# Performance work log

Measured on AMD Instinct MI355X. Metric: run time of the kernel, lower is better.

Reference implementation:

```python
import jax, jax.numpy as jnp
import numpy as np

D = 256
N = 8192
M = 8192


def setup_inputs() -> dict:
    key = jax.random.key(0)
    k1, k2, k3 = jax.random.split(key, 3)
    query = jax.random.normal(k1, (N, D), dtype=jnp.float32)
    context = jax.random.normal(k2, (M, D), dtype=jnp.float32)
    # nn.Linear(D, D, bias=False) weight, stored torch-style as [out, in]
    W = jax.random.normal(k3, (D, D), dtype=jnp.float32) * (1.0 / np.sqrt(D))
    return {"query": query, "context": context, "W": W}


def reference(query, context, W):
    # L2-normalize rows (matches torch: x / x.norm(dim=1)[:, None])
    query_norm = query / jnp.linalg.norm(query, axis=1, keepdims=True)
    context_norm = context / jnp.linalg.norm(context, axis=1, keepdims=True)
    cos_sim = query_norm @ context_norm.T                     # [N, M]
    q_lin = query @ W.T                                        # linear_in, no bias
    attn = jax.nn.softmax(q_lin @ context.T, axis=-1)          # [N, M]
    # vectorized form of the per-row torch.dot loop: row-wise dot then mean
    y_pred = jnp.sum(attn * cos_sim) / attn.shape[0]
    return jax.nn.relu(y_pred)
```

## Files before the change

### kernel.cpp

```cpp
#include <hip/hip_runtime.h>
#include <hip/hip_bf16.h>

#define DEV __device__ __forceinline__

using bf16x8 = __attribute__((ext_vector_type(8))) short;
using f32x4  = __attribute__((ext_vector_type(4))) float;
using u16x4  = __attribute__((ext_vector_type(4))) unsigned short;
using i32x4  = __attribute__((ext_vector_type(4))) int;
using i32x8  = __attribute__((ext_vector_type(8))) int;

constexpr int N = 8192;
constexpr int M = 8192;
constexpr int D = 256;
constexpr int ROWB = D * 2;
constexpr int ROW8 = D;
constexpr int MSPLIT = 8;
constexpr int SPLEN = M / MSPLIT;
constexpr int KVB = 32;
constexpr int NCHUNK = SPLEN / KVB;
constexpr int CH8  = KVB * ROW8;
constexpr int CHB64 = 64 * ROWB;
constexpr float L2E = 1.4426950408889634f;
constexpr float SBIAS = -40.0f;
constexpr unsigned SCL1 = 0x7F7F7F7Fu;

DEV unsigned short f2bf(float f) {
  unsigned int x = __float_as_uint(f);
  return (unsigned short)((x + 0x7fffu + ((x >> 16) & 1u)) >> 16);
}

DEV int pk_fp8x4(float a, float b, float c, float d) {
  int p = __builtin_amdgcn_cvt_pk_fp8_f32(a, b, 0, false);
  p = __builtin_amdgcn_cvt_pk_fp8_f32(c, d, p, true);
  return p;
}

DEV f32x4 MFMA(bf16x8 a, bf16x8 b, f32x4 c) {
  return __builtin_amdgcn_mfma_f32_16x16x32_bf16(a, b, c, 0, 0, 0);
}

DEV f32x4 SMFMA(i32x8 a, i32x8 b, f32x4 c) {
  return __builtin_amdgcn_mfma_scale_f32_16x16x128_f8f6f4(
      a, b, c, 0, 0, 0, SCL1, 0, SCL1);
}

DEV void gload_lds16(const void* g, void* l) {
  __builtin_amdgcn_global_load_lds(
      (const __attribute__((address_space(1))) unsigned int*)g,
      (__attribute__((address_space(3))) unsigned int*)l, 16, 0, 0);
}

DEV void stage_group(const char* gbase, char* lds, int tid, int grp) {
  int wid = tid >> 6;
#pragma unroll
  for (int j = 0; j < 2; ++j) {
    int r    = grp * 2 + j;
    int o    = r * 4096 + tid * 16;
    int row  = o >> 9;
    int colb = o & 511;
    int scol = colb ^ ((row & 7) << 4);
    gload_lds16(gbase + row * ROWB + scol, lds + r * 4096 + wid * 1024);
  }
}

DEV bf16x8 lds_frag(const char* lds, int row, int colb) {
  int addr = row * 512 + (colb ^ ((row & 7) << 4));
  return *(const bf16x8*)(lds + addr);
}

DEV void stage_chunk8(const char* gbase, char* lds, int tid) {
  int o    = tid * 16;
  int row  = o >> 8;
  int colb = o & 255;
  int scol = colb ^ ((row & 7) << 4);
  gload_lds16(gbase + row * ROW8 + scol, lds + o);
}

#define VMW(n) asm volatile("s_waitcnt vmcnt(" #n ")" ::: "memory")

__global__ __launch_bounds__(256) void prep_kernel(
    const float* __restrict__ query, const float* __restrict__ context,
    const float* __restrict__ W, unsigned short* __restrict__ qb,
    unsigned char* __restrict__ qn8, unsigned char* __restrict__ c8,
    unsigned short* __restrict__ wb, float* __restrict__ rnc) {
  int tid = threadIdx.x;
  int lane = tid & 63, wid = tid >> 6;
  int row = blockIdx.x * 4 + wid;
  const float* src;
  if (row < N) src = query + (size_t)row * D;
  else if (row < N + M) src = context + (size_t)(row - N) * D;
  else src = W + (size_t)(row - N - M) * D;
  f32x4 v = *(const f32x4*)(src + lane * 4);
  float s = v[0] * v[0] + v[1] * v[1] + v[2] * v[2] + v[3] * v[3];
#pragma unroll
  for (int m = 1; m <= 32; m <<= 1) s += __shfl_xor(s, m);
  float rn = rsqrtf(s);
  if (row < N) {
    u16x4 raw;
#pragma unroll
    for (int i = 0; i < 4; ++i) raw[i] = f2bf(v[i]);
    *(u16x4*)(qb + (size_t)row * D + lane * 4) = raw;
    float sc = rn * 16.0f;
    *(int*)(qn8 + (size_t)row * D + lane * 4) =
        pk_fp8x4(v[0] * sc, v[1] * sc, v[2] * sc, v[3] * sc);
  } else if (row < N + M) {
    int r = row - N;
    *(int*)(c8 + (size_t)r * D + lane * 4) = pk_fp8x4(v[0], v[1], v[2], v[3]);
    if (lane == 0) rnc[r] = rn * 0.0625f;
  } else {
    int r = row - N - M;
    u16x4 raw;
#pragma unroll
    for (int i = 0; i < 4; ++i) raw[i] = f2bf(v[i]);
    *(u16x4*)(wb + (size_t)r * D + lane * 4) = raw;
  }
}

__global__ __launch_bounds__(256, 2) void qlin_kernel(
    const unsigned short* __restrict__ qb, const unsigned short* __restrict__ wb,
    unsigned char* __restrict__ ql8) {
  __shared__ alignas(16) char ldsW[CHB64];
  int tid = threadIdx.x;
  int lane = tid & 63, wid = tid >> 6;
  int l15 = lane & 15, g = lane >> 4;
  int q0 = blockIdx.x * 32 + (wid & 1) * 16;
  int cthalf = wid >> 1;
  bf16x8 bq[8];
#pragma unroll
  for (int k = 0; k < 8; ++k)
    bq[k] = *(const bf16x8*)((const char*)qb + (size_t)(q0 + l15) * ROWB + k * 64 + g * 16);
  for (int ch = 0; ch < 4; ++ch) {
    __syncthreads();
#pragma unroll
    for (int grp = 0; grp < 4; ++grp)
      stage_group((const char*)wb + (size_t)ch * CHB64, ldsW, tid, grp);
    __syncthreads();
    f32x4 z = {0.f, 0.f, 0.f, 0.f};
    f32x4 acc[2] = {z, z};
#pragma unroll
    for (int k = 0; k < 8; ++k)
#pragma unroll
      for (int j = 0; j < 2; ++j) {
        int ct = cthalf * 2 + j;
        bf16x8 a = lds_frag(ldsW, ct * 16 + l15, k * 64 + g * 16);
        acc[j] = MFMA(a, bq[k], acc[j]);
      }
#pragma unroll
    for (int j = 0; j < 2; ++j) {
      int ct = cthalf * 2 + j;
      int q = q0 + l15;
      int o = ch * 64 + ct * 16 + g * 4;
      *(int*)(ql8 + (size_t)q * D + o) =
          pk_fp8x4(acc[j][0] * L2E, acc[j][1] * L2E, acc[j][2] * L2E, acc[j][3] * L2E);
    }
  }
}

__global__ __launch_bounds__(512, 4) void attn_kernel(
    const unsigned char* __restrict__ ql8, const unsigned char* __restrict__ qn8,
    const unsigned char* __restrict__ c8, const float* __restrict__ rnc,
    float* __restrict__ lP, float* __restrict__ tP) {
  __shared__ alignas(16) char ldsC[3 * CH8];
  __shared__ alignas(16) float ldsR[SPLEN];
  int tid = threadIdx.x;
  int lane = tid & 63;
  int wid = tid >> 6;
  int l15 = lane & 15, g = lane >> 4;
  int bq = blockIdx.x & 63;
  int sp = blockIdx.x >> 6;
  int q0 = bq * 128 + wid * 16;

  i32x8 bl[2], bn[2];
#pragma unroll
  for (int t = 0; t < 2; ++t) {
    const char* qrow = (const char*)ql8 + (size_t)(q0 + l15) * D;
    const char* nrow = (const char*)qn8 + (size_t)(q0 + l15) * D;
    i32x4 lo = *(const i32x4*)(qrow + t * 128 + g * 32);
    i32x4 hi = *(const i32x4*)(qrow + t * 128 + g * 32 + 16);
    bl[t] = i32x8{lo[0], lo[1], lo[2], lo[3], hi[0], hi[1], hi[2], hi[3]};
    lo = *(const i32x4*)(nrow + t * 128 + g * 32);
    hi = *(const i32x4*)(nrow + t * 128 + g * 32 + 16);
    bn[t] = i32x8{lo[0], lo[1], lo[2], lo[3], hi[0], hi[1], hi[2], hi[3]};
  }

  float lrun = 0.f, trun = 0.f;

  const char*  cbase = (const char*)c8 + (size_t)sp * SPLEN * ROW8;
  const float* rbase = rnc + sp * SPLEN;

  if (tid < SPLEN / 4) *(f32x4*)(ldsR + tid * 4) = *(const f32x4*)(rbase + tid * 4);
  __syncthreads();

  auto compute_phase = [&](const char* pr, char* pw, const char* gs,
                           bool stg, int ch, int ct) {
    int row = ct * 16 + l15;
    i32x8 a[2];
#pragma unroll
    for (int t = 0; t < 2; ++t) {
      int c0b = (t * 128 + g * 32) ^ ((row & 7) << 4);
      int c1b = (t * 128 + g * 32 + 16) ^ ((row & 7) << 4);
      i32x4 lo = *(const i32x4*)(pr + row * 256 + c0b);
      i32x4 hi = *(const i32x4*)(pr + row * 256 + c1b);
      a[t] = i32x8{lo[0], lo[1], lo[2], lo[3], hi[0], hi[1], hi[2], hi[3]};
    }
    f32x4 rv = *(const f32x4*)(ldsR + ch * KVB + ct * 16 + g * 4);
    if (stg && ct == 0) stage_chunk8(gs, pw, tid);
    f32x4 s = {SBIAS, SBIAS, SBIAS, SBIAS};
    f32x4 c = {0.f, 0.f, 0.f, 0.f};
    __builtin_amdgcn_s_setprio(1);
    s = SMFMA(a[0], bl[0], s);
    c = SMFMA(a[0], bn[0], c);
    s = SMFMA(a[1], bl[1], s);
    c = SMFMA(a[1], bn[1], c);
    __builtin_amdgcn_s_setprio(0);
    float ls = 0.f, ts = 0.f;
    f32x4 p;
#pragma unroll
    for (int r = 0; r < 4; ++r) {
      p[r] = __builtin_amdgcn_exp2f(s[r]);
      ls += p[r];
    }
#pragma unroll
    for (int r = 0; r < 4; ++r) ts += p[r] * (c[r] * rv[r]);
    lrun += ls; trun += ts;
  };

  stage_chunk8(cbase, ldsC, tid);
  stage_chunk8(cbase + CH8, ldsC + CH8, tid);
  VMW(1);
  __builtin_amdgcn_s_barrier();
  __builtin_amdgcn_sched_barrier(0);

  const char* pr = ldsC;
  const char* pn = ldsC + CH8;
  char*       pw = ldsC + 2 * CH8;

#pragma unroll 1
  for (int ch = 0; ch < NCHUNK; ++ch) {
    const char* gs = cbase + (size_t)(ch + 2) * CH8;
    bool stg = (ch + 2 < NCHUNK);
    compute_phase(pr, pw, gs, stg, ch, 0);
    compute_phase(pr, pw, gs, stg, ch, 1);
    if (ch + 1 < NCHUNK) {
      if (stg) { VMW(1); } else { VMW(0); }
      __builtin_amdgcn_s_barrier();
      __builtin_amdgcn_sched_barrier(0);
    }
    const char* t = pr; pr = pn; pn = pw; pw = (char*)t;
  }

  {
    float lsum = lrun; lsum += __shfl_xor(lsum, 16); lsum += __shfl_xor(lsum, 32);
    float tsum = trun; tsum += __shfl_xor(tsum, 16); tsum += __shfl_xor(tsum, 32);
    if (g == 0) {
      int i = q0 + l15;
      lP[sp * N + i] = lsum;
      tP[sp * N + i] = tsum;
    }
  }
}

__global__ __launch_bounds__(256) void rowred_kernel(
    const float* __restrict__ lP, const float* __restrict__ tP,
    float* __restrict__ part) {
  __shared__ float red[4];
  int tid = threadIdx.x;
  int i = blockIdx.x * 256 + tid;
  float L = 0.f, T = 0.f;
#pragma unroll
  for (int s = 0; s < MSPLIT; ++s) {
    L += lP[s * N + i];
    T += tP[s * N + i];
  }
  float acc = T / L;
#pragma unroll
  for (int m = 1; m <= 32; m <<= 1) acc += __shfl_xor(acc, m);
  int lane = tid & 63, wid = tid >> 6;
  if (lane == 0) red[wid] = acc;
  __syncthreads();
  if (tid == 0) part[blockIdx.x] = red[0] + red[1] + red[2] + red[3];
}

__global__ __launch_bounds__(64) void final_kernel(
    const float* __restrict__ part, float* __restrict__ out) {
  int tid = threadIdx.x;
  float v = (tid < 32) ? part[tid] : 0.f;
#pragma unroll
  for (int m = 1; m <= 32; m <<= 1) v += __shfl_xor(v, m);
  if (tid == 0) out[0] = fmaxf(v / (float)N, 0.f);
}

extern "C" void kernel_launch(void* const* d_in, const int* in_sizes, int n_in,
                              void* d_out, int out_size, void* d_ws, size_t ws_size,
                              hipStream_t stream) {
  const float* query   = (const float*)d_in[0];
  const float* context = (const float*)d_in[1];
  const float* W       = (const float*)d_in[2];
  float* out = (float*)d_out;
  char* ws = (char*)d_ws;

  unsigned short* qb  = (unsigned short*)(ws);
  unsigned short* wb  = (unsigned short*)(ws + (4u << 20));
  unsigned char*  qn8 = (unsigned char*)(ws + (4u << 20) + (256u << 10));
  unsigned char*  c8  = qn8 + (2u << 20);
  unsigned char*  ql8 = c8 + (2u << 20);
  float* rnc = (float*)(ql8 + (2u << 20));
  float* lP  = rnc + (64u << 10) / 4;
  float* tP  = lP + MSPLIT * N;
  float* part = tP + MSPLIT * N;

  hipLaunchKernelGGL(prep_kernel, dim3((N + M + D) / 4), dim3(256), 0, stream,
                     query, context, W, qb, qn8, c8, wb, rnc);
  hipLaunchKernelGGL(qlin_kernel, dim3(N / 32), dim3(256), 0, stream, qb, wb, ql8);
  hipLaunchKernelGGL(attn_kernel, dim3(64 * MSPLIT), dim3(512), 0, stream,
                     ql8, qn8, c8, rnc, lP, tP);
  hipLaunchKernelGGL(rowred_kernel, dim3(N / 256), dim3(256), 0, stream,
                     lP, tP, part);
  hipLaunchKernelGGL(final_kernel, dim3(1), dim3(64), 0, stream, part, out);
}
```

Baseline: 57.51 us.

## Process two query tiles per wave to reuse each context fragment from LDS

Each wave now handles 32 query rows (two 16-row tiles) rather than 16. Every context fragment read from LDS therefore feeds twice as many MFMAs. The M dimension is split 16 ways instead of 8, which keeps the grid at 512 blocks. This halves LDS reads and context staging per unit of work, at the cost of more registers for the query fragments and twice as many partial sums for the row reduction.

Measured after the change: 72.47 us. +26.0%, slower.

```diff
diff --git a/kernel.cpp b/kernel.cpp
--- a/kernel.cpp
+++ b/kernel.cpp
@@ -14,7 +14,7 @@
 constexpr int D = 256;
 constexpr int ROWB = D * 2;
 constexpr int ROW8 = D;
-constexpr int MSPLIT = 8;
+constexpr int MSPLIT = 16;
 constexpr int SPLEN = M / MSPLIT;
 constexpr int KVB = 32;
 constexpr int NCHUNK = SPLEN / KVB;
@@ -166,24 +166,27 @@
   int lane = tid & 63;
   int wid = tid >> 6;
   int l15 = lane & 15, g = lane >> 4;
-  int bq = blockIdx.x & 63;
-  int sp = blockIdx.x >> 6;
-  int q0 = bq * 128 + wid * 16;
-
-  i32x8 bl[2], bn[2];
-#pragma unroll
-  for (int t = 0; t < 2; ++t) {
-    const char* qrow = (const char*)ql8 + (size_t)(q0 + l15) * D;
-    const char* nrow = (const char*)qn8 + (size_t)(q0 + l15) * D;
-    i32x4 lo = *(const i32x4*)(qrow + t * 128 + g * 32);
-    i32x4 hi = *(const i32x4*)(qrow + t * 128 + g * 32 + 16);
-    bl[t] = i32x8{lo[0], lo[1], lo[2], lo[3], hi[0], hi[1], hi[2], hi[3]};
-    lo = *(const i32x4*)(nrow + t * 128 + g * 32);
-    hi = *(const i32x4*)(nrow + t * 128 + g * 32 + 16);
-    bn[t] = i32x8{lo[0], lo[1], lo[2], lo[3], hi[0], hi[1], hi[2], hi[3]};
-  }
-
-  float lrun = 0.f, trun = 0.f;
+  int bq = blockIdx.x & 31;
+  int sp = blockIdx.x >> 5;
+  int q0 = bq * 256 + wid * 32;
+
+  i32x8 bl[2][2], bn[2][2];
+#pragma unroll
+  for (int qt = 0; qt < 2; ++qt)
+#pragma unroll
+    for (int t = 0; t < 2; ++t) {
+      const char* qrow = (const char*)ql8 + (size_t)(q0 + qt * 16 + l15) * D;
+      const char* nrow = (const char*)qn8 + (size_t)(q0 + qt * 16 + l15) * D;
+      i32x4 lo = *(const i32x4*)(qrow + t * 128 + g * 32);
+      i32x4 hi = *(const i32x4*)(qrow + t * 128 + g * 32 + 16);
+      bl[qt][t] = i32x8{lo[0], lo[1], lo[2], lo[3], hi[0], hi[1], hi[2], hi[3]};
+      lo = *(const i32x4*)(nrow + t * 128 + g * 32);
+      hi = *(const i32x4*)(nrow + t * 128 + g * 32 + 16);
+      bn[qt][t] = i32x8{lo[0], lo[1], lo[2], lo[3], hi[0], hi[1], hi[2], hi[3]};
+    }
+
+  float lrun[2] = {0.f, 0.f};
+  float trun[2] = {0.f, 0.f};
 
   const char*  cbase = (const char*)c8 + (size_t)sp * SPLEN * ROW8;
   const float* rbase = rnc + sp * SPLEN;
@@ -205,24 +208,32 @@
     }
     f32x4 rv = *(const f32x4*)(ldsR + ch * KVB + ct * 16 + g * 4);
     if (stg && ct == 0) stage_chunk8(gs, pw, tid);
-    f32x4 s = {SBIAS, SBIAS, SBIAS, SBIAS};
-    f32x4 c = {0.f, 0.f, 0.f, 0.f};
+    f32x4 s0 = {SBIAS, SBIAS, SBIAS, SBIAS}, s1 = s0;
+    f32x4 c0 = {0.f, 0.f, 0.f, 0.f}, c1 = c0;
     __builtin_amdgcn_s_setprio(1);
-    s = SMFMA(a[0], bl[0], s);
-    c = SMFMA(a[0], bn[0], c);
-    s = SMFMA(a[1], bl[1], s);
-    c = SMFMA(a[1], bn[1], c);
+    s0 = SMFMA(a[0], bl[0][0], s0);
+    s1 = SMFMA(a[0], bl[1][0], s1);
+    c0 = SMFMA(a[0], bn[0][0], c0);
+    c1 = SMFMA(a[0], bn[1][0], c1);
+    s0 = SMFMA(a[1], bl[0][1], s0);
+    s1 = SMFMA(a[1], bl[1][1], s1);
+    c0 = SMFMA(a[1], bn[0][1], c0);
+    c1 = SMFMA(a[1], bn[1][1], c1);
     __builtin_amdgcn_s_setprio(0);
-    float ls = 0.f, ts = 0.f;
-    f32x4 p;
+    float ls0 = 0.f, ts0 = 0.f, ls1 = 0.f, ts1 = 0.f;
+    f32x4 p0, p1;
 #pragma unroll
     for (int r = 0; r < 4; ++r) {
-      p[r] = __builtin_amdgcn_exp2f(s[r]);
-      ls += p[r];
-    }
-#pragma unroll
-    for (int r = 0; r < 4; ++r) ts += p[r] * (c[r] * rv[r]);
-    lrun += ls; trun += ts;
+      p0[r] = __builtin_amdgcn_exp2f(s0[r]);
+      p1[r] = __builtin_amdgcn_exp2f(s1[r]);
+      ls0 += p0[r]; ls1 += p1[r];
+    }
+#pragma unroll
+    for (int r = 0; r < 4; ++r) {
+      ts0 += p0[r] * (c0[r] * rv[r]);
+      ts1 += p1[r] * (c1[r] * rv[r]);
+    }
+    lrun[0] += ls0; trun[0] += ts0; lrun[1] += ls1; trun[1] += ts1;
   };
 
   stage_chunk8(cbase, ldsC, tid);
@@ -249,11 +260,12 @@
     const char* t = pr; pr = pn; pn = pw; pw = (char*)t;
   }
 
-  {
-    float lsum = lrun; lsum += __shfl_xor(lsum, 16); lsum += __shfl_xor(lsum, 32);
-    float tsum = trun; tsum += __shfl_xor(tsum, 16); tsum += __shfl_xor(tsum, 32);
+#pragma unroll
+  for (int qt = 0; qt < 2; ++qt) {
+    float lsum = lrun[qt]; lsum += __shfl_xor(lsum, 16); lsum += __shfl_xor(lsum, 32);
+    float tsum = trun[qt]; tsum += __shfl_xor(tsum, 16); tsum += __shfl_xor(tsum, 32);
     if (g == 0) {
-      int i = q0 + l15;
+      int i = q0 + qt * 16 + l15;
       lP[sp * N + i] = lsum;
       tP[sp * N + i] = tsum;
     }
@@ -312,7 +324,7 @@
   hipLaunchKernelGGL(prep_kernel, dim3((N + M + D) / 4), dim3(256), 0, stream,
                      query, context, W, qb, qn8, c8, wb, rnc);
   hipLaunchKernelGGL(qlin_kernel, dim3(N / 32), dim3(256), 0, stream, qb, wb, ql8);
-  hipLaunchKernelGGL(attn_kernel, dim3(64 * MSPLIT), dim3(512), 0, stream,
+  hipLaunchKernelGGL(attn_kernel, dim3(32 * MSPLIT), dim3(512), 0, stream,
                      ql8, qn8, c8, rnc, lP, tP);
   hipLaunchKernelGGL(rowred_kernel, dim3(N / 256), dim3(256), 0, stream,
                      lP, tP, part);
```
